# Optimization experiments

Hardware: AMD Instinct MI355X
Metric: run time of the kernel (lower is better)

The kernel has to match this reference:

```python
import jax, jax.numpy as jnp
import numpy as np

VOCAB, EMB, UNITS, B, S = 32000, 256, 512, 32, 512


def _lstm_scan(x_bse, h0, c0, W, U, b):
    """Keras-order LSTM (gates i,f,g,o). x_bse: [B,S,E]. Returns (out [B,S,U], hT, cT)."""
    # Precompute input projections for all timesteps: [B,S,4U] -> [S,B,4U]
    zx = jnp.einsum('bse,eu->bsu', x_bse, W) + b
    zx = jnp.swapaxes(zx, 0, 1)

    def step(carry, zt):
        h, c = carry
        z = zt + h @ U  # [B,4U]
        i, f, g, o = jnp.split(z, 4, axis=-1)
        i = jax.nn.sigmoid(i)
        f = jax.nn.sigmoid(f)
        g = jnp.tanh(g)
        o = jax.nn.sigmoid(o)
        c = f * c + i * g
        h = o * jnp.tanh(c)
        return (h, c), h

    (hT, cT), hs = jax.lax.scan(step, (h0, c0), zx)
    return jnp.swapaxes(hs, 0, 1), hT, cT


def setup_inputs() -> dict:
    key = jax.random.key(0)
    ks = jax.random.split(key, 8)
    g = 0.05
    inp = {
        'x': jax.random.randint(ks[0], (B, S), 0, VOCAB),
        'fh': jnp.zeros((B, UNITS), jnp.float32),
        'fc': jnp.zeros((B, UNITS), jnp.float32),
        'bh': jnp.zeros((B, UNITS), jnp.float32),
        'bc': jnp.zeros((B, UNITS), jnp.float32),
        'emb': jax.random.normal(ks[1], (VOCAB, EMB), jnp.float32) * g,
        'Wf': jax.random.normal(ks[2], (EMB, 4 * UNITS), jnp.float32) * g,
        'Uf': jax.random.normal(ks[3], (UNITS, 4 * UNITS), jnp.float32) * g,
        'bf': jnp.zeros((4 * UNITS,), jnp.float32),
        'Wb': jax.random.normal(ks[4], (EMB, 4 * UNITS), jnp.float32) * g,
        'Ub': jax.random.normal(ks[5], (UNITS, 4 * UNITS), jnp.float32) * g,
        'bb': jnp.zeros((4 * UNITS,), jnp.float32),
    }
    return inp


def reference(x, fh, fc, bh, bc, emb, Wf, Uf, bf, Wb, Ub, bb):
    xe = emb[x]  # [B,S,E] embedding lookup
    # Forward direction
    out_f, fhT, fcT = _lstm_scan(xe, fh, fc, Wf, Uf, bf)
    # Backward direction: process reversed sequence, then re-reverse outputs
    out_b_rev, bhT, bcT = _lstm_scan(xe[:, ::-1, :], bh, bc, Wb, Ub, bb)
    out_b = out_b_rev[:, ::-1, :]
    output = jnp.concatenate([out_f, out_b], axis=-1)  # [B,S,2U]
    return output, fhT, fcT, bhT, bcT
```

## Files before the change

### kernel.cpp

```cpp
#include <hip/hip_runtime.h>

#define SEQ   512
#define BATCH 32
#define EMBD  256
#define UNITS 512
#define G4    2048
#define NW1   128
#define NW2   32
#define UPW   16
#define HSTR  520
#define NTHR  512

typedef short  short8 __attribute__((ext_vector_type(8)));
typedef float  f32x4  __attribute__((ext_vector_type(4)));
typedef unsigned int u32x4 __attribute__((ext_vector_type(4)));
typedef unsigned int u32x2 __attribute__((ext_vector_type(2)));

static constexpr unsigned long long ZX2_OFF   = 0ull;
static constexpr unsigned long long ZX2_BYTES = 2ull * SEQ * NW1 * BATCH * 16 * 2;
static constexpr unsigned long long HB_OFF    = ZX2_OFF + ZX2_BYTES;
static constexpr unsigned long long HB_BYTES  = 2ull * SEQ * BATCH * UNITS * 2;
static constexpr unsigned long long FLG_OFF   = HB_OFF + HB_BYTES;
static constexpr unsigned long long FLG_BYTES = 4096;
static constexpr unsigned long long SF_OFF    = FLG_OFF + FLG_BYTES;
static constexpr unsigned long long SF_BYTES  = 2ull * SEQ * NW2 * 4;

__device__ __forceinline__ unsigned short f2bf(float f) {
  unsigned int u = __float_as_uint(f);
  u = (u + 0x7FFFu + ((u >> 16) & 1u)) >> 16;
  return (unsigned short)u;
}
__device__ __forceinline__ float bf2f(unsigned short s) {
  return __uint_as_float(((unsigned int)s) << 16);
}
__device__ __forceinline__ unsigned sent2(unsigned w) {
  return (unsigned)(((w & 0xFFFFu) == 0xFFFFu) | ((w >> 16) == 0xFFFFu));
}
__device__ __forceinline__ unsigned chk4(u32x4 g) {
  return sent2(g[0]) | sent2(g[1]) | sent2(g[2]) | sent2(g[3]);
}

__global__ __launch_bounds__(256)
void k_zx(const int* __restrict__ x, const float* __restrict__ emb,
          const float* __restrict__ Wf, const float* __restrict__ bf,
          const float* __restrict__ Wb, const float* __restrict__ bb,
          unsigned short* __restrict__ zx2)
{
  const int nb  = blockIdx.x;
  const int mb  = blockIdx.y;
  const int dir = blockIdx.z;
  const float* __restrict__ W    = dir ? Wb : Wf;
  const float* __restrict__ bias = dir ? bb : bf;
  const int tid = threadIdx.x;
  const int M0 = mb * 64, N0 = nb * 64;

  __shared__ __align__(16) float Ast[32][68];
  __shared__ __align__(16) float Bs [32][68];
  __shared__ int tok[64];

  if (tid < 64) {
    int m = M0 + tid;
    int t = m >> 5, b = m & 31;
    int s = dir ? (SEQ - 1 - t) : t;
    tok[tid] = x[b * SEQ + s];
  }

  float acc[4][4];
  #pragma unroll
  for (int r = 0; r < 4; ++r)
    #pragma unroll
    for (int c = 0; c < 4; ++c) acc[r][c] = 0.f;

  const int mq = tid >> 4, nq = tid & 15;

  for (int kb = 0; kb < 8; ++kb) {
    __syncthreads();
    {
      int m = tid >> 2, q = tid & 3;
      const float* src = emb + (size_t)tok[m] * EMBD + kb * 32 + q * 8;
      float4 v0 = *(const float4*)src;
      float4 v1 = *(const float4*)(src + 4);
      int k0 = q * 8;
      Ast[k0+0][m] = v0.x; Ast[k0+1][m] = v0.y; Ast[k0+2][m] = v0.z; Ast[k0+3][m] = v0.w;
      Ast[k0+4][m] = v1.x; Ast[k0+5][m] = v1.y; Ast[k0+6][m] = v1.z; Ast[k0+7][m] = v1.w;
    }
    {
      int k = tid >> 3, q = tid & 7;
      const float* src = W + (size_t)(kb*32 + k) * G4 + N0 + q * 8;
      float4 w0 = *(const float4*)src;
      float4 w1 = *(const float4*)(src + 4);
      *(float4*)&Bs[k][q*8]     = w0;
      *(float4*)&Bs[k][q*8 + 4] = w1;
    }
    __syncthreads();
    #pragma unroll 8
    for (int k = 0; k < 32; ++k) {
      float4 a  = *(const float4*)&Ast[k][mq*4];
      float4 bv = *(const float4*)&Bs[k][nq*4];
      acc[0][0] += a.x*bv.x; acc[0][1] += a.x*bv.y; acc[0][2] += a.x*bv.z; acc[0][3] += a.x*bv.w;
      acc[1][0] += a.y*bv.x; acc[1][1] += a.y*bv.y; acc[1][2] += a.y*bv.z; acc[1][3] += a.y*bv.w;
      acc[2][0] += a.z*bv.x; acc[2][1] += a.z*bv.y; acc[2][2] += a.z*bv.z; acc[2][3] += a.z*bv.w;
      acc[3][0] += a.w*bv.x; acc[3][1] += a.w*bv.y; acc[3][2] += a.w*bv.z; acc[3][3] += a.w*bv.w;
    }
  }

  float4 bs4 = *(const float4*)(bias + N0 + nq*4);
  const int g = N0 >> 9;
  const int u = (N0 & 511) + nq * 4;
  const int w = u >> 2;
  #pragma unroll
  for (int r = 0; r < 4; ++r) {
    int m = M0 + mq*4 + r;
    int t = m >> 5, b = m & 31;
    unsigned short p0 = f2bf(acc[r][0] + bs4.x);
    unsigned short p1 = f2bf(acc[r][1] + bs4.y);
    unsigned short p2 = f2bf(acc[r][2] + bs4.z);
    unsigned short p3 = f2bf(acc[r][3] + bs4.w);
    uint2 pk;
    pk.x = (unsigned)p0 | ((unsigned)p1 << 16);
    pk.y = (unsigned)p2 | ((unsigned)p3 << 16);
    size_t off = ((((size_t)dir*SEQ + t)*NW1 + w)*BATCH + b)*16 + g*4;
    *(uint2*)(zx2 + off) = pk;
  }
}

__global__ __launch_bounds__(NTHR, 2)
void k_rec2(const float* __restrict__ fh, const float* __restrict__ fc,
            const float* __restrict__ bh, const float* __restrict__ bc,
            const float* __restrict__ Uf, const float* __restrict__ Ub,
            const unsigned short* __restrict__ zx2,
            unsigned short* __restrict__ hring_all,
            int* __restrict__ claim, int* __restrict__ sflag,
            float* __restrict__ out)
{
  const int tid = threadIdx.x;
  __shared__ int s_slot, s_loc;

  if (tid == 0) {
    unsigned xcc;
    asm volatile("s_getreg_b32 %0, hwreg(HW_REG_XCC_ID)" : "=s"(xcc));
    int slot = -1;
    if (xcc < 2) {
      int base = (int)xcc * NW2;
      for (int i = 0; i < NW2 && slot < 0; ++i)
        if (atomicCAS(&claim[base + i], 0, 1) == 0) slot = base + i;
    }
    if (slot < 0) {
      for (int sp = 0; sp < 96; ++sp) __builtin_amdgcn_s_sleep(8);
      for (int i = 0; i < 2 * NW2 && slot < 0; ++i)
        if (atomicCAS(&claim[i], 0, 1) == 0) slot = i;
    }
    s_slot = slot;
    s_loc  = (slot >= 0 && (unsigned)(slot >> 5) == xcc) ? 1 : 0;
  }
  __syncthreads();
  const int slot = s_slot;
  if (slot < 0) return;
  const int loc = s_loc;
  const int dir = slot >> 5;
  const int w   = slot & (NW2 - 1);
  const int u0  = w * UPW;
  const int l   = tid & 63;
  const int wid = tid >> 6;
  const int mt  = wid & 1;
  const int ct  = wid >> 1;

  const float* __restrict__ U  = dir ? Ub : Uf;
  const float* __restrict__ h0 = dir ? bh : fh;
  const float* __restrict__ c0 = dir ? bc : fc;

  __shared__ __align__(16) unsigned short hs[BATCH * HSTR];

  unsigned short* __restrict__ hring = hring_all + (size_t)dir * SEQ * BATCH * UNITS;
  int* __restrict__ flg = sflag + (size_t)dir * SEQ * NW2;
  const unsigned short* __restrict__ zxd =
      zx2 + ((size_t)dir * SEQ) * (NW1 * BATCH * 16);

  const int krow = (l >> 4) * 8;
  const size_t gcol = (size_t)((l & 15) >> 2) * 512 + u0 + ct * 4 + (l & 3);
  short8 uhi[16], ulo[16];
  #pragma unroll
  for (int s = 0; s < 16; ++s) {
    const float* up = U + (size_t)(s * 32 + krow) * G4 + gcol;
    short8 hi8, lo8;
    #pragma unroll
    for (int j = 0; j < 8; ++j) {
      float uv = up[(size_t)j * G4];
      unsigned short h16 = f2bf(uv);
      float rem = uv - bf2f(h16);
      hi8[j] = (short)h16;
      lo8[j] = (short)f2bf(rem);
    }
    uhi[s] = hi8; ulo[s] = lo8;
  }

  float c_old[4];
  #pragma unroll
  for (int r = 0; r < 4; ++r) {
    int b_r = 16 * mt + (l >> 4) * 4 + r;
    c_old[r] = c0[(size_t)b_r * UNITS + u0 + ct * 4 + (l & 3)];
  }

  {
    int r = tid >> 4, cq = tid & 15;
    const float* src = h0 + (size_t)r * UNITS;
    #pragma unroll
    for (int i = 0; i < 4; ++i) {
      int c = i * 16 + cq;
      float4 v0 = *(const float4*)(src + c * 8);
      float4 v1 = *(const float4*)(src + c * 8 + 4);
      short8 pk;
      pk[0]=(short)f2bf(v0.x); pk[1]=(short)f2bf(v0.y);
      pk[2]=(short)f2bf(v0.z); pk[3]=(short)f2bf(v0.w);
      pk[4]=(short)f2bf(v1.x); pk[5]=(short)f2bf(v1.y);
      pk[6]=(short)f2bf(v1.z); pk[7]=(short)f2bf(v1.w);
      *(short8*)(&hs[r * HSTR + c * 8]) = pk;
    }
  }
  __syncthreads();

  const int arow  = 16 * mt + (l & 15);
  const unsigned short* hsrow = hs + arow * HSTR;
  const int agrp0 = l >> 4;
  const int sr = tid >> 4, scq = tid & 15;
  unsigned short* const hs_dst = hs + sr * HSTR + scq * 8;
  const bool isg = ((l & 15) >> 2) == 2;
  const float An = isg ? 2.f : 1.f;
  const float Cn = isg ? -1.f : 0.f;
  const float Bn = isg ? -2.f : -1.f;
  const size_t ZXT = (size_t)NW1 * BATCH * 16;
  const size_t zbase = ((size_t)(4 * w + ct) * BATCH + 16 * mt + (l >> 4) * 4) * 16
                       + ((l & 15) >> 2) * 4 + (l & 3);

  unsigned short zx_cur[4];
  #pragma unroll
  for (int r = 0; r < 4; ++r) zx_cur[r] = zxd[zbase + r * 16];

  for (int t = 0; t < SEQ; ++t) {
    if (t > 0) {
      asm volatile("s_waitcnt vmcnt(0)" ::: "memory");
      {
        const int* fpl = flg + (size_t)(t - 1) * NW2 + (l & 31);
        unsigned v; int guard = 0;
        for (;;) {
          if ((guard & 3) == 3)
            asm volatile("global_load_dword %0, %1, off sc0 sc1\n\ts_waitcnt vmcnt(0)"
                         : "=v"(v) : "v"(fpl) : "memory");
          else
            asm volatile("global_load_dword %0, %1, off sc0\n\ts_waitcnt vmcnt(0)"
                         : "=v"(v) : "v"(fpl) : "memory");
          __builtin_amdgcn_sched_barrier(0);
          if (__ballot(v != 0) == ~0ull || ++guard >= (1 << 20)) break;
          __builtin_amdgcn_s_sleep(1);
        }
      }
      const unsigned short* src =
          hring + ((size_t)(t - 1) * BATCH + sr) * UNITS + scq * 8;
      u32x4 g0, g1, g2, g3;
      asm volatile("global_load_dwordx4 %0, %1, off sc0"            : "=&v"(g0) : "v"(src) : "memory");
      asm volatile("global_load_dwordx4 %0, %1, off offset:256 sc0" : "=&v"(g1) : "v"(src) : "memory");
      asm volatile("global_load_dwordx4 %0, %1, off offset:512 sc0" : "=&v"(g2) : "v"(src) : "memory");
      asm volatile("global_load_dwordx4 %0, %1, off offset:768 sc0" : "=&v"(g3) : "v"(src) : "memory");
      asm volatile("s_waitcnt vmcnt(0)" : "+v"(g0), "+v"(g1), "+v"(g2), "+v"(g3));
      __builtin_amdgcn_sched_barrier(0);
      unsigned b0 = chk4(g0), b1 = chk4(g1), b2 = chk4(g2), b3 = chk4(g3);
      int guard = 0;
      while ((b0 | b1 | b2 | b3) && ++guard < (1 << 20)) {
        __builtin_amdgcn_s_sleep(1);
        if (guard & 1) {
          if (b0) asm volatile("global_load_dwordx4 %0, %1, off sc0 sc1"            : "=&v"(g0) : "v"(src) : "memory");
          if (b1) asm volatile("global_load_dwordx4 %0, %1, off offset:256 sc0 sc1" : "=&v"(g1) : "v"(src) : "memory");
          if (b2) asm volatile("global_load_dwordx4 %0, %1, off offset:512 sc0 sc1" : "=&v"(g2) : "v"(src) : "memory");
          if (b3) asm volatile("global_load_dwordx4 %0, %1, off offset:768 sc0 sc1" : "=&v"(g3) : "v"(src) : "memory");
        } else {
          if (b0) asm volatile("global_load_dwordx4 %0, %1, off sc0"            : "=&v"(g0) : "v"(src) : "memory");
          if (b1) asm volatile("global_load_dwordx4 %0, %1, off offset:256 sc0" : "=&v"(g1) : "v"(src) : "memory");
          if (b2) asm volatile("global_load_dwordx4 %0, %1, off offset:512 sc0" : "=&v"(g2) : "v"(src) : "memory");
          if (b3) asm volatile("global_load_dwordx4 %0, %1, off offset:768 sc0" : "=&v"(g3) : "v"(src) : "memory");
        }
        asm volatile("s_waitcnt vmcnt(0)" : "+v"(g0), "+v"(g1), "+v"(g2), "+v"(g3));
        __builtin_amdgcn_sched_barrier(0);
        b0 = chk4(g0); b1 = chk4(g1); b2 = chk4(g2); b3 = chk4(g3);
      }
      *(u32x4*)(hs_dst      ) = g0;
      *(u32x4*)(hs_dst + 128) = g1;
      *(u32x4*)(hs_dst + 256) = g2;
      *(u32x4*)(hs_dst + 384) = g3;
      __syncthreads();
    }

    f32x4 accA = {0.f, 0.f, 0.f, 0.f};
    f32x4 accB = {0.f, 0.f, 0.f, 0.f};
    #pragma unroll
    for (int s = 0; s < 16; ++s) {
      short8 a = *(const short8*)(hsrow + (4 * s + agrp0) * 8);
      accA = __builtin_amdgcn_mfma_f32_16x16x32_bf16(a, uhi[s], accA, 0, 0, 0);
      accB = __builtin_amdgcn_mfma_f32_16x16x32_bf16(a, ulo[s], accB, 0, 0, 0);
    }

    float vv[4];
    #pragma unroll
    for (int r = 0; r < 4; ++r) {
      float z = accA[r] + accB[r] + bf2f(zx_cur[r]);
      float e = __expf(Bn * z);
      vv[r] = An * __builtin_amdgcn_rcpf(1.f + e) + Cn;
    }
    float hn[4], cn[4];
    unsigned pk0[4], pk1[4];
    #pragma unroll
    for (int r = 0; r < 4; ++r) {
      float wv = __shfl_xor(vv[r], 8);
      float x1 = __shfl_xor(vv[r], 4);
      float x2 = __shfl_xor(wv,    4);
      cn[r] = x1 * c_old[r] + vv[r] * wv;
      c_old[r] = cn[r];
      float e2 = __expf(-2.f * cn[r]);
      float th = 2.f * __builtin_amdgcn_rcpf(1.f + e2) - 1.f;
      hn[r] = x2 * th;
      unsigned hb = (unsigned)f2bf(hn[r]);
      unsigned d  = (hb & 0xFFFFu) | (__shfl_xor((int)hb, 1) << 16);
      unsigned d2 = (unsigned)__shfl_xor((int)d, 2);
      pk0[r] = d; pk1[r] = d2;
    }

    if (t < SEQ - 1) {
      if ((l & 15) == 0) {
        #pragma unroll
        for (int r = 0; r < 4; ++r) {
          int b_r = 16 * mt + (l >> 4) * 4 + r;
          unsigned short* dst = hring + ((size_t)t * BATCH + b_r) * UNITS + u0 + ct * 4;
          u32x2 pk; pk[0] = pk0[r]; pk[1] = pk1[r];
          if (loc)
            asm volatile("global_store_dwordx2 %0, %1, off sc0"
                         :: "v"(dst), "v"(pk) : "memory");
          else
            asm volatile("global_store_dwordx2 %0, %1, off sc0 sc1"
                         :: "v"(dst), "v"(pk) : "memory");
        }
      }
    }
    __builtin_amdgcn_sched_barrier(0);

    unsigned short zx_nxt[4] = {0, 0, 0, 0};
    if (t + 1 < SEQ) {
      #pragma unroll
      for (int r = 0; r < 4; ++r)
        zx_nxt[r] = zxd[(size_t)(t + 1) * ZXT + zbase + r * 16];
    }
    __builtin_amdgcn_sched_barrier(0);

    if ((l & 15) < 4) {
      int sidx = dir ? (SEQ - 1 - t) : t;
      #pragma unroll
      for (int r = 0; r < 4; ++r) {
        int b_r = 16 * mt + (l >> 4) * 4 + r;
        size_t oi = ((size_t)b_r * SEQ + sidx) * 1024 + dir * 512 + u0 + ct * 4 + (l & 3);
        __builtin_nontemporal_store(hn[r], &out[oi]);
      }
      if (t == SEQ - 1) {
        size_t base = (size_t)BATCH * SEQ * 1024;
        #pragma unroll
        for (int r = 0; r < 4; ++r) {
          int b_r = 16 * mt + (l >> 4) * 4 + r;
          size_t o1 = base + (size_t)(2*dir  ) * BATCH * UNITS + (size_t)b_r * UNITS + u0 + ct * 4 + (l & 3);
          size_t o2 = base + (size_t)(2*dir+1) * BATCH * UNITS + (size_t)b_r * UNITS + u0 + ct * 4 + (l & 3);
          __builtin_nontemporal_store(hn[r], &out[o1]);
          __builtin_nontemporal_store(cn[r], &out[o2]);
        }
      }
    }
    __builtin_amdgcn_sched_barrier(0);

    if (t < SEQ - 1) {
      asm volatile("s_waitcnt vmcnt(8)" ::: "memory");
      if (tid == 0) {
        int* fdst = flg + (size_t)t * NW2 + w;
        unsigned one = 1u;
        if (loc)
          asm volatile("global_store_dword %0, %1, off sc0"
                       :: "v"(fdst), "v"(one) : "memory");
        else
          asm volatile("global_store_dword %0, %1, off sc0 sc1"
                       :: "v"(fdst), "v"(one) : "memory");
      }
    }

    #pragma unroll
    for (int r = 0; r < 4; ++r) zx_cur[r] = zx_nxt[r];
  }
}

extern "C" void kernel_launch(void* const* d_in, const int* in_sizes, int n_in,
                              void* d_out, int out_size, void* d_ws, size_t ws_size,
                              hipStream_t stream)
{
  const int*   x   = (const int*)  d_in[0];
  const float* fh  = (const float*)d_in[1];
  const float* fc  = (const float*)d_in[2];
  const float* bh  = (const float*)d_in[3];
  const float* bc  = (const float*)d_in[4];
  const float* emb = (const float*)d_in[5];
  const float* Wf  = (const float*)d_in[6];
  const float* Uf  = (const float*)d_in[7];
  const float* bf  = (const float*)d_in[8];
  const float* Wb  = (const float*)d_in[9];
  const float* Ub  = (const float*)d_in[10];
  const float* bb  = (const float*)d_in[11];
  float* out = (float*)d_out;

  if (ws_size < SF_OFF + SF_BYTES) return;

  unsigned short* zx2   = (unsigned short*)((char*)d_ws + ZX2_OFF);
  unsigned short* hring = (unsigned short*)((char*)d_ws + HB_OFF);
  int*            claim = (int*)((char*)d_ws + FLG_OFF);
  int*            sflag = (int*)((char*)d_ws + SF_OFF);

  hipMemsetAsync(hring, 0xFF, HB_BYTES, stream);
  hipMemsetAsync(claim, 0, FLG_BYTES + SF_BYTES, stream);
  k_zx  <<<dim3(32, 256, 2), 256, 0, stream>>>(x, emb, Wf, bf, Wb, bb, zx2);
  k_rec2<<<dim3(256), NTHR, 0, stream>>>(fh, fc, bh, bc, Uf, Ub, zx2, hring, claim, sflag, out);
}
```

Baseline: 1.918 ms.

## Stage LSTM outputs in LDS and signal step flags earlier

Per-step hidden outputs are now buffered in a double-banked LDS array. Every 8 timesteps they are written to global memory as vectorised 16-byte nontemporal stores, instead of scattered scalar stores each step. The step-completion flag store now follows the h-ring store immediately, and the vmcnt waits are dropped. The next-step zx prefetch is hoisted ahead of the barrier, shortening the serial critical path between recurrence steps. Dropping the waits risks memory-ordering problems between the h-ring data and the flag seen by other blocks.

```diff
diff --git a/kernel.cpp b/kernel.cpp
--- a/kernel.cpp
+++ b/kernel.cpp
@@ -170,6 +170,7 @@
   const float* __restrict__ c0 = dir ? bc : fc;
 
   __shared__ __align__(16) unsigned short hs[BATCH * HSTR];
+  __shared__ __align__(16) float obuf[2][8][BATCH][16];
 
   unsigned short* __restrict__ hring = hring_all + (size_t)dir * SEQ * BATCH * UNITS;
   int* __restrict__ flg = sflag + (size_t)dir * SEQ * NW2;
@@ -231,6 +232,7 @@
   const size_t ZXT = (size_t)NW1 * BATCH * 16;
   const size_t zbase = ((size_t)(4 * w + ct) * BATCH + 16 * mt + (l >> 4) * 4) * 16
                        + ((l & 15) >> 2) * 4 + (l & 3);
+  const int bj = wid, bb_ = (tid >> 1) & 31, uqp = tid & 1;
 
   unsigned short zx_cur[4];
   #pragma unroll
@@ -238,7 +240,6 @@
 
   for (int t = 0; t < SEQ; ++t) {
     if (t > 0) {
-      asm volatile("s_waitcnt vmcnt(0)" ::: "memory");
       {
         const int* fpl = flg + (size_t)(t - 1) * NW2 + (l & 31);
         unsigned v; int guard = 0;
@@ -286,8 +287,29 @@
       *(u32x4*)(hs_dst + 128) = g1;
       *(u32x4*)(hs_dst + 256) = g2;
       *(u32x4*)(hs_dst + 384) = g3;
-      __syncthreads();
-    }
+
+      if ((t & 7) == 0 && t >= 8) {
+        int tb = t - 8, bank = ((t - 8) >> 3) & 1;
+        int tj = tb + bj;
+        int sidx = dir ? (SEQ - 1 - tj) : tj;
+        const f32x4* sp = (const f32x4*)&obuf[bank][bj][bb_][uqp * 8];
+        f32x4 v0 = sp[0];
+        f32x4 v1 = sp[1];
+        float* dst = out + ((size_t)bb_ * SEQ + sidx) * 1024 + dir * 512 + u0 + uqp * 8;
+        __builtin_nontemporal_store(v0, (f32x4*)dst);
+        __builtin_nontemporal_store(v1, (f32x4*)(dst + 4));
+      }
+      __builtin_amdgcn_sched_barrier(0);
+    }
+
+    unsigned short zx_nxt[4] = {0, 0, 0, 0};
+    if (t + 1 < SEQ) {
+      #pragma unroll
+      for (int r = 0; r < 4; ++r)
+        zx_nxt[r] = zxd[(size_t)(t + 1) * ZXT + zbase + r * 16];
+    }
+    __builtin_amdgcn_sched_barrier(0);
+    if (t > 0) __syncthreads();
 
     f32x4 accA = {0.f, 0.f, 0.f, 0.f};
     f32x4 accB = {0.f, 0.f, 0.f, 0.f};
@@ -338,25 +360,25 @@
                          :: "v"(dst), "v"(pk) : "memory");
         }
       }
+      __builtin_amdgcn_sched_barrier(0);
+      if (tid == 0) {
+        int* fdst = flg + (size_t)t * NW2 + w;
+        unsigned one = 1u;
+        if (loc)
+          asm volatile("global_store_dword %0, %1, off sc0"
+                       :: "v"(fdst), "v"(one) : "memory");
+        else
+          asm volatile("global_store_dword %0, %1, off sc0 sc1"
+                       :: "v"(fdst), "v"(one) : "memory");
+      }
     }
     __builtin_amdgcn_sched_barrier(0);
 
-    unsigned short zx_nxt[4] = {0, 0, 0, 0};
-    if (t + 1 < SEQ) {
+    if ((l & 15) < 4) {
+      int jj = t & 7, bank = (t >> 3) & 1;
       #pragma unroll
       for (int r = 0; r < 4; ++r)
-        zx_nxt[r] = zxd[(size_t)(t + 1) * ZXT + zbase + r * 16];
-    }
-    __builtin_amdgcn_sched_barrier(0);
-
-    if ((l & 15) < 4) {
-      int sidx = dir ? (SEQ - 1 - t) : t;
-      #pragma unroll
-      for (int r = 0; r < 4; ++r) {
-        int b_r = 16 * mt + (l >> 4) * 4 + r;
-        size_t oi = ((size_t)b_r * SEQ + sidx) * 1024 + dir * 512 + u0 + ct * 4 + (l & 3);
-        __builtin_nontemporal_store(hn[r], &out[oi]);
-      }
+        obuf[bank][jj][16 * mt + (l >> 4) * 4 + r][ct * 4 + (l & 3)] = hn[r];
       if (t == SEQ - 1) {
         size_t base = (size_t)BATCH * SEQ * 1024;
         #pragma unroll
@@ -369,24 +391,22 @@
         }
       }
     }
-    __builtin_amdgcn_sched_barrier(0);
-
-    if (t < SEQ - 1) {
-      asm volatile("s_waitcnt vmcnt(8)" ::: "memory");
-      if (tid == 0) {
-        int* fdst = flg + (size_t)t * NW2 + w;
-        unsigned one = 1u;
-        if (loc)
-          asm volatile("global_store_dword %0, %1, off sc0"
-                       :: "v"(fdst), "v"(one) : "memory");
-        else
-          asm volatile("global_store_dword %0, %1, off sc0 sc1"
-                       :: "v"(fdst), "v"(one) : "memory");
-      }
-    }
 
     #pragma unroll
     for (int r = 0; r < 4; ++r) zx_cur[r] = zx_nxt[r];
+  }
+
+  __syncthreads();
+  {
+    int tb = SEQ - 8, bank = ((SEQ - 8) >> 3) & 1;
+    int tj = tb + bj;
+    int sidx = dir ? (SEQ - 1 - tj) : tj;
+    const f32x4* sp = (const f32x4*)&obuf[bank][bj][bb_][uqp * 8];
+    f32x4 v0 = sp[0];
+    f32x4 v1 = sp[1];
+    float* dst = out + ((size_t)bb_ * SEQ + sidx) * 1024 + dir * 512 + u0 + uqp * 8;
+    __builtin_nontemporal_store(v0, (f32x4*)dst);
+    __builtin_nontemporal_store(v1, (f32x4*)(dst + 4));
   }
 }
 
```

New measurement: 1.945 ms. Within noise of the previous version (+1.4%).
